# Kernel tuning notes

Hardware: AMD Instinct MI355X
Metric: run time of the kernel (lower is better)

Reference implementation:

```python
import jax, jax.numpy as jnp
import numpy as np

N, NS, C, S = 262144, 8, 32, 8  # points, nsample, out_channels, share_channels
EPS = 1e-5

def _bn(x, g, b, axes):
    m = jnp.mean(x, axis=axes, keepdims=True)
    v = jnp.mean((x - m) ** 2, axis=axes, keepdims=True)
    return g * (x - m) * jax.lax.rsqrt(v + EPS) + b

def setup_inputs() -> dict:
    key = jax.random.key(0)
    ks = jax.random.split(key, 16)
    lin = lambda k, i, o: (jax.random.normal(k, (o, i), jnp.float32) / np.sqrt(i)).astype(jnp.float32)
    return {
        'p': jax.random.normal(ks[0], (N, 3), jnp.float32) * 10.0,
        'x': jax.random.normal(ks[1], (N, C), jnp.float32),
        'idx': jax.random.randint(ks[2], (N, NS), 0, N, jnp.int32),
        'Wq': lin(ks[3], C, C), 'bq': jnp.zeros((C,), jnp.float32),
        'Wk': lin(ks[4], C, C), 'bk': jnp.zeros((C,), jnp.float32),
        'Wv': lin(ks[5], C, C), 'bv': jnp.zeros((C,), jnp.float32),
        'Wp1': lin(ks[6], 3, 3), 'bp1': jnp.zeros((3,), jnp.float32),
        'gp': jnp.ones((3,), jnp.float32), 'bp': jnp.zeros((3,), jnp.float32),
        'Wp2': lin(ks[7], 3, C), 'bp2': jnp.zeros((C,), jnp.float32),
        'gw1': jnp.ones((C,), jnp.float32), 'bw1': jnp.zeros((C,), jnp.float32),
        'Ww1': lin(ks[8], C, C // S), 'bww1': jnp.zeros((C // S,), jnp.float32),
        'gw2': jnp.ones((C // S,), jnp.float32), 'bw2': jnp.zeros((C // S,), jnp.float32),
        'Ww2': lin(ks[9], C // S, C // S), 'bww2': jnp.zeros((C // S,), jnp.float32),
    }

def reference(p, x, idx, Wq, bq, Wk, bk, Wv, bv, Wp1, bp1, gp, bp, Wp2, bp2,
              gw1, bw1, Ww1, bww1, gw2, bw2, Ww2, bww2):
    n = x.shape[0]
    q = x @ Wq.T + bq                      # (n, C)
    k = x @ Wk.T + bk
    v = x @ Wv.T + bv
    # queryandgroup: gather neighbors, relative xyz (use_xyz=True for key path)
    p_r = p[idx] - p[:, None, :]           # (n, ns, 3)
    kg = k[idx]                            # (n, ns, C)
    vg = v[idx]                            # (n, ns, C)
    # linear_p: Linear(3,3) -> BN(3) (over n, ns) -> ReLU -> Linear(3, C)
    p_r = p_r @ Wp1.T + bp1
    p_r = jax.nn.relu(_bn(p_r, gp, bp, (0, 1)))
    p_r = p_r @ Wp2.T + bp2                # (n, ns, C)
    # out_channels // mid_channels == 1, so the .view(...).sum(2) is identity
    w = kg - q[:, None, :] + p_r           # (n, ns, C)
    # linear_w: BN(C) -> ReLU -> Linear(C, C//S) -> BN(C//S) -> ReLU -> Linear
    w = jax.nn.relu(_bn(w, gw1, bw1, (0, 1)))
    w = w @ Ww1.T + bww1                   # (n, ns, C//S)
    w = jax.nn.relu(_bn(w, gw2, bw2, (0, 1)))
    w = w @ Ww2.T + bww2
    w = jax.nn.softmax(w, axis=1)          # softmax over nsample
    # grouped weighted sum: (n, ns, S, C//S) * (n, ns, 1, C//S)
    out = ((vg + p_r).reshape(n, NS, S, C // S) * w[:, :, None, :]).sum(1)
    return out.reshape(n, C)
```

## Files before the change

### kernel.cpp

```cpp
#include <hip/hip_runtime.h>
#include <hip/hip_bf16.h>

#define NPTS   262144
#define NSAMP  8
#define NPAIR  (NPTS * NSAMP)
#define EPSV   1e-5f
#define INVCNT (1.0f / (float)NPAIR)
#define GSTAT  1024

typedef __hip_bfloat16 bf16;

template <typename T> __device__ __forceinline__ float cvt(T v);
template <> __device__ __forceinline__ float cvt<float>(float v) { return v; }
template <> __device__ __forceinline__ float cvt<bf16>(bf16 v) { return __bfloat162float(v); }

template <typename T> __device__ __forceinline__ T f2t(float v);
template <> __device__ __forceinline__ float f2t<float>(float v) { return v; }
template <> __device__ __forceinline__ bf16  f2t<bf16>(float v)  { return __float2bfloat16(v); }

__global__ void k_detect(const unsigned int* __restrict__ xw, int* __restrict__ flag)
{
    if (threadIdx.x == 0 && blockIdx.x == 0) {
        int cnt = 0;
        for (int i = 0; i < 256; ++i) {
            const unsigned int w = xw[i];
            const unsigned int e = (w >> 7) & 0xFF;
            if (e >= 110 && e <= 132) ++cnt;
        }
        flag[0] = (cnt >= 128) ? 0 : 1;
    }
}

template <typename T>
__global__ __launch_bounds__(256) void k_qkv(
    const T* __restrict__ x,
    const T* __restrict__ Wq, const T* __restrict__ bq,
    const T* __restrict__ Wk, const T* __restrict__ bk,
    const T* __restrict__ Wv, const T* __restrict__ bv,
    float* __restrict__ q, float* __restrict__ k, float* __restrict__ v,
    const int* __restrict__ flag, const int want)
{
    if (flag[0] != want) return;
    __shared__ float Wt[3][32][32];
    __shared__ float xs[8][32];
    const int t = threadIdx.x;
    for (int e = t; e < 1024; e += 256) {
        const int c = e >> 5, j = e & 31;
        Wt[0][j][c] = cvt<T>(Wq[e]);
        Wt[1][j][c] = cvt<T>(Wk[e]);
        Wt[2][j][c] = cvt<T>(Wv[e]);
    }
    __syncthreads();
    const int c = t & 31, pi = t >> 5;
    const float bqv = cvt<T>(bq[c]), bkv = cvt<T>(bk[c]), bvv = cvt<T>(bv[c]);
    const int base0 = blockIdx.x * 256;
    for (int it = 0; it < 32; ++it) {
        const int base = base0 + it * 8;
        __syncthreads();
        xs[t >> 5][t & 31] = cvt<T>(x[base * 32 + t]);
        __syncthreads();
        float aq = bqv, ak = bkv, av = bvv;
#pragma unroll
        for (int j = 0; j < 32; ++j) {
            const float xv = xs[pi][j];
            aq += Wt[0][j][c] * xv;
            ak += Wt[1][j][c] * xv;
            av += Wt[2][j][c] * xv;
        }
        const int o = (base + pi) * 32 + c;
        q[o] = aq; k[o] = ak; v[o] = av;
    }
}

template <typename T>
__global__ __launch_bounds__(256) void k_pr1(
    const T* __restrict__ p, const int* __restrict__ idx,
    const T* __restrict__ Wp1, const T* __restrict__ bp1,
    float* __restrict__ pr1, float* __restrict__ P1,
    const int* __restrict__ flag, const int want)
{
    if (flag[0] != want) return;
    float W[3][3], B[3];
#pragma unroll
    for (int a = 0; a < 3; ++a) {
        B[a] = cvt<T>(bp1[a]);
#pragma unroll
        for (int d = 0; d < 3; ++d) W[a][d] = cvt<T>(Wp1[a * 3 + d]);
    }
    const int t = threadIdx.x;
    const int base = blockIdx.x * 2048;
    float s[3] = {0.f, 0.f, 0.f}, ss[3] = {0.f, 0.f, 0.f};
    for (int it = 0; it < 2048; it += 256) {
        const int pid = base + it + t;
        const int i = pid >> 3;
        const int nj = idx[pid];
        const float d0 = cvt<T>(p[nj * 3 + 0]) - cvt<T>(p[i * 3 + 0]);
        const float d1 = cvt<T>(p[nj * 3 + 1]) - cvt<T>(p[i * 3 + 1]);
        const float d2 = cvt<T>(p[nj * 3 + 2]) - cvt<T>(p[i * 3 + 2]);
#pragma unroll
        for (int a = 0; a < 3; ++a) {
            const float r = W[a][0] * d0 + W[a][1] * d1 + W[a][2] * d2 + B[a];
            pr1[pid * 3 + a] = r;
            s[a] += r; ss[a] += r * r;
        }
    }
#pragma unroll
    for (int o = 32; o > 0; o >>= 1) {
#pragma unroll
        for (int a = 0; a < 3; ++a) { s[a] += __shfl_down(s[a], o); ss[a] += __shfl_down(ss[a], o); }
    }
    __shared__ float red[4][16];
    const int wid = t >> 6, lane = t & 63;
    if (lane == 0) {
#pragma unroll
        for (int u = 0; u < 16; ++u) red[wid][u] = 0.f;
#pragma unroll
        for (int a = 0; a < 3; ++a) { red[wid][a] = s[a]; red[wid][8 + a] = ss[a]; }
    }
    __syncthreads();
    if (t < 16) P1[blockIdx.x * 16 + t] = red[0][t] + red[1][t] + red[2][t] + red[3][t];
}

template <typename T, int NC_, int NP_>
__global__ __launch_bounds__(1024) void k_fin(
    const float* __restrict__ P, const int nblocks,
    const T* __restrict__ g, const T* __restrict__ b,
    float* __restrict__ A, float* __restrict__ Cc,
    const int* __restrict__ flag, const int want)
{
    if (flag[0] != want) return;
    constexpr int COLS = 2 * NP_;
    constexpr int GRP  = 1024 / COLS;
    const int t = threadIdx.x;
    const int c = t % COLS;
    const int gi = t / COLS;
    float acc = 0.f;
    for (int r = gi; r < nblocks; r += GRP) acc += P[r * COLS + c];
    __shared__ float red[1024];
    red[t] = acc;
    __syncthreads();
#pragma unroll
    for (int s = GRP >> 1; s > 0; s >>= 1) {
        if (gi < s) red[t] += red[t + s * COLS];
        __syncthreads();
    }
    if (t < NC_) {
        const float m = red[t] * INVCNT;
        const float var = red[NP_ + t] * INVCNT - m * m;
        const float a = cvt<T>(g[t]) * rsqrtf(var + EPSV);
        A[t] = a;
        Cc[t] = cvt<T>(b[t]) - a * m;
    }
}

template <typename T>
__global__ __launch_bounds__(256) void k_bn2stat(
    const int* __restrict__ idx, const float* __restrict__ pr1,
    const float* __restrict__ q, const float* __restrict__ k,
    const T* __restrict__ Wp2, const T* __restrict__ bp2,
    const float* __restrict__ coef, float* __restrict__ P2,
    const int* __restrict__ flag, const int want)
{
    if (flag[0] != want) return;
    const int t = threadIdx.x;
    const int c = t & 31;
    const float a10 = coef[0], a11 = coef[1], a12 = coef[2];
    const float c10 = coef[8], c11 = coef[9], c12 = coef[10];
    const float w0 = cvt<T>(Wp2[c * 3 + 0]), w1 = cvt<T>(Wp2[c * 3 + 1]), w2 = cvt<T>(Wp2[c * 3 + 2]);
    const float bb = cvt<T>(bp2[c]);
    float s = 0.f, ss = 0.f;
    const int base = blockIdx.x * 2048;
    for (int it = 0; it < 2048; it += 8) {
        const int pid = base + it + (t >> 5);
        const int i = pid >> 3;
        const int nj = idx[pid];
        const float h0 = fmaxf(a10 * pr1[pid * 3 + 0] + c10, 0.f);
        const float h1 = fmaxf(a11 * pr1[pid * 3 + 1] + c11, 0.f);
        const float h2 = fmaxf(a12 * pr1[pid * 3 + 2] + c12, 0.f);
        const float pr2 = w0 * h0 + w1 * h1 + w2 * h2 + bb;
        const float wp = k[nj * 32 + c] - q[i * 32 + c] + pr2;
        s += wp; ss += wp * wp;
    }
    s += __shfl_down(s, 32); ss += __shfl_down(ss, 32);
    __shared__ float red[4][64];
    const int wid = t >> 6, lane = t & 63;
    if (lane < 32) { red[wid][lane] = s; red[wid][32 + lane] = ss; }
    __syncthreads();
    if (t < 64) P2[blockIdx.x * 64 + t] = red[0][t] + red[1][t] + red[2][t] + red[3][t];
}

template <typename T>
__global__ __launch_bounds__(256) void k_w1(
    const int* __restrict__ idx, const float* __restrict__ pr1,
    const float* __restrict__ q, const float* __restrict__ k,
    const T* __restrict__ Wp2, const T* __restrict__ bp2,
    const T* __restrict__ Ww1, const T* __restrict__ bww1,
    const float* __restrict__ coef, float* __restrict__ w1out, float* __restrict__ P3,
    const int* __restrict__ flag, const int want)
{
    if (flag[0] != want) return;
    __shared__ float sWp2[32][3], sbp2[32], sW1[4][32], sb1[4], sa2[32], sc2[32];
    const int t = threadIdx.x;
    if (t < 32) {
        sWp2[t][0] = cvt<T>(Wp2[t * 3 + 0]);
        sWp2[t][1] = cvt<T>(Wp2[t * 3 + 1]);
        sWp2[t][2] = cvt<T>(Wp2[t * 3 + 2]);
        sbp2[t] = cvt<T>(bp2[t]);
        sa2[t] = coef[16 + t];
        sc2[t] = coef[48 + t];
    }
    if (t < 4) sb1[t] = cvt<T>(bww1[t]);
    if (t < 128) sW1[t >> 5][t & 31] = cvt<T>(Ww1[t]);
    __syncthreads();
    const float a10 = coef[0], a11 = coef[1], a12 = coef[2];
    const float c10 = coef[8], c11 = coef[9], c12 = coef[10];
    float s[4] = {0.f, 0.f, 0.f, 0.f}, ss[4] = {0.f, 0.f, 0.f, 0.f};
    const int base = blockIdx.x * 2048;
    for (int it = 0; it < 2048; it += 256) {
        const int pid = base + it + t;
        const int i = pid >> 3;
        const int nj = idx[pid];
        const float h0 = fmaxf(a10 * pr1[pid * 3 + 0] + c10, 0.f);
        const float h1 = fmaxf(a11 * pr1[pid * 3 + 1] + c11, 0.f);
        const float h2 = fmaxf(a12 * pr1[pid * 3 + 2] + c12, 0.f);
        float acc[4] = {sb1[0], sb1[1], sb1[2], sb1[3]};
        const float* krow = k + nj * 32;
        const float* qrow = q + i * 32;
#pragma unroll
        for (int cc = 0; cc < 32; ++cc) {
            const float pr2 = sWp2[cc][0] * h0 + sWp2[cc][1] * h1 + sWp2[cc][2] * h2 + sbp2[cc];
            const float wp = krow[cc] - qrow[cc] + pr2;
            const float hh = fmaxf(sa2[cc] * wp + sc2[cc], 0.f);
            acc[0] += sW1[0][cc] * hh;
            acc[1] += sW1[1][cc] * hh;
            acc[2] += sW1[2][cc] * hh;
            acc[3] += sW1[3][cc] * hh;
        }
#pragma unroll
        for (int u = 0; u < 4; ++u) {
            w1out[pid * 4 + u] = acc[u];
            s[u] += acc[u]; ss[u] += acc[u] * acc[u];
        }
    }
#pragma unroll
    for (int o = 32; o > 0; o >>= 1) {
#pragma unroll
        for (int u = 0; u < 4; ++u) { s[u] += __shfl_down(s[u], o); ss[u] += __shfl_down(ss[u], o); }
    }
    __shared__ float red[4][8];
    const int wid = t >> 6, lane = t & 63;
    if (lane == 0) {
#pragma unroll
        for (int u = 0; u < 4; ++u) { red[wid][u] = s[u]; red[wid][4 + u] = ss[u]; }
    }
    __syncthreads();
    if (t < 8) P3[blockIdx.x * 8 + t] = red[0][t] + red[1][t] + red[2][t] + red[3][t];
}

template <typename T>
__global__ __launch_bounds__(256) void k_out(
    const int* __restrict__ idx, const float* __restrict__ pr1,
    const float* __restrict__ v, const float* __restrict__ w1in,
    const T* __restrict__ Wp2, const T* __restrict__ bp2,
    const T* __restrict__ Ww2, const T* __restrict__ bww2,
    const float* __restrict__ coef, T* __restrict__ out,
    const int* __restrict__ flag, const int want)
{
    if (flag[0] != want) return;
    const int t = threadIdx.x;
    const int c = t & 31, pi = t >> 5;
    const float a10 = coef[0], a11 = coef[1], a12 = coef[2];
    const float c10 = coef[8], c11 = coef[9], c12 = coef[10];
    const float wA = cvt<T>(Wp2[c * 3 + 0]), wB = cvt<T>(Wp2[c * 3 + 1]), wC = cvt<T>(Wp2[c * 3 + 2]);
    const float bb = cvt<T>(bp2[c]);
    const int tq = c & 3;
    float a3[4], c3[4], W2r[4];
#pragma unroll
    for (int u = 0; u < 4; ++u) {
        a3[u] = coef[80 + u]; c3[u] = coef[88 + u];
        W2r[u] = cvt<T>(Ww2[tq * 4 + u]);
    }
    const float b2r = cvt<T>(bww2[tq]);
    const int base0 = blockIdx.x * 256;
    for (int it = 0; it < 32; ++it) {
        const int i = base0 + it * 8 + pi;
        float lg[8];
#pragma unroll
        for (int j = 0; j < 8; ++j) {
            const float* wr = w1in + (i * 8 + j) * 4;
            float l = b2r;
#pragma unroll
            for (int u = 0; u < 4; ++u) l += W2r[u] * fmaxf(a3[u] * wr[u] + c3[u], 0.f);
            lg[j] = l;
        }
        float m = lg[0];
#pragma unroll
        for (int j = 1; j < 8; ++j) m = fmaxf(m, lg[j]);
        float sum = 0.f;
#pragma unroll
        for (int j = 0; j < 8; ++j) { lg[j] = __expf(lg[j] - m); sum += lg[j]; }
        const float inv = 1.f / sum;
        float acc = 0.f;
#pragma unroll
        for (int j = 0; j < 8; ++j) {
            const int pid = i * 8 + j;
            const int nj = idx[pid];
            const float h0 = fmaxf(a10 * pr1[pid * 3 + 0] + c10, 0.f);
            const float h1 = fmaxf(a11 * pr1[pid * 3 + 1] + c11, 0.f);
            const float h2 = fmaxf(a12 * pr1[pid * 3 + 2] + c12, 0.f);
            const float pr2 = wA * h0 + wB * h1 + wC * h2 + bb;
            acc += (v[nj * 32 + c] + pr2) * (lg[j] * inv);
        }
        out[i * 32 + c] = f2t<T>(acc);
    }
}

template <typename T>
static void launch_pipeline(void* const* d_in, void* d_out, float* ws,
                            int* flag, const int want, hipStream_t stream)
{
    const T*   p    = (const T*)d_in[0];
    const T*   x    = (const T*)d_in[1];
    const int* idx  = (const int*)d_in[2];
    const T*   Wq   = (const T*)d_in[3];
    const T*   bq   = (const T*)d_in[4];
    const T*   Wk   = (const T*)d_in[5];
    const T*   bk   = (const T*)d_in[6];
    const T*   Wv   = (const T*)d_in[7];
    const T*   bv   = (const T*)d_in[8];
    const T*   Wp1  = (const T*)d_in[9];
    const T*   bp1  = (const T*)d_in[10];
    const T*   gp   = (const T*)d_in[11];
    const T*   bp   = (const T*)d_in[12];
    const T*   Wp2  = (const T*)d_in[13];
    const T*   bp2  = (const T*)d_in[14];
    const T*   gw1  = (const T*)d_in[15];
    const T*   bw1  = (const T*)d_in[16];
    const T*   Ww1  = (const T*)d_in[17];
    const T*   bww1 = (const T*)d_in[18];
    const T*   gw2  = (const T*)d_in[19];
    const T*   bw2  = (const T*)d_in[20];
    const T*   Ww2  = (const T*)d_in[21];
    const T*   bww2 = (const T*)d_in[22];
    T* out = (T*)d_out;

    float* coef = ws + 16;
    float* P1   = ws + 128;
    float* P2   = P1 + GSTAT * 16;
    float* P3   = P2 + GSTAT * 64;
    float* q    = ws + 131072;
    float* k    = q  + (size_t)NPTS * 32;
    float* v    = k  + (size_t)NPTS * 32;
    float* pr1  = v  + (size_t)NPTS * 32;
    float* w1   = pr1 + (size_t)NPAIR * 3;

    k_qkv<T><<<1024, 256, 0, stream>>>(x, Wq, bq, Wk, bk, Wv, bv, q, k, v, flag, want);
    k_pr1<T><<<GSTAT, 256, 0, stream>>>(p, idx, Wp1, bp1, pr1, P1, flag, want);
    k_fin<T, 3, 8><<<1, 1024, 0, stream>>>(P1, GSTAT, gp, bp, coef + 0, coef + 8, flag, want);
    k_bn2stat<T><<<GSTAT, 256, 0, stream>>>(idx, pr1, q, k, Wp2, bp2, coef, P2, flag, want);
    k_fin<T, 32, 32><<<1, 1024, 0, stream>>>(P2, GSTAT, gw1, bw1, coef + 16, coef + 48, flag, want);
    k_w1<T><<<GSTAT, 256, 0, stream>>>(idx, pr1, q, k, Wp2, bp2, Ww1, bww1, coef, w1, P3, flag, want);
    k_fin<T, 4, 4><<<1, 1024, 0, stream>>>(P3, GSTAT, gw2, bw2, coef + 80, coef + 88, flag, want);
    k_out<T><<<1024, 256, 0, stream>>>(idx, pr1, v, w1, Wp2, bp2, Ww2, bww2, coef, out, flag, want);
}

extern "C" void kernel_launch(void* const* d_in, const int* in_sizes, int n_in,
                              void* d_out, int out_size, void* d_ws, size_t ws_size,
                              hipStream_t stream)
{
    float* ws = (float*)d_ws;
    int* flag = (int*)ws;

    k_detect<<<1, 64, 0, stream>>>((const unsigned int*)d_in[1], flag);
    launch_pipeline<bf16>(d_in, d_out, ws, flag, 0, stream);
    launch_pipeline<float>(d_in, d_out, ws, flag, 1, stream);
}
```

Measured before the change: 519.0 us.

## Double grid sizes to 2048 blocks and unroll bn2stat gathers by four

Doubles the block count for every per-point kernel, halving the work per block, and moves the workspace offset for q so the larger partial-stat buffers fit. k_bn2stat now issues four independent idx/pr1/k/q loads per iteration before using them, to expose more memory-level parallelism on the random gathers. Several index computations are widened to size_t. The risk is more partial sums for the single-block finalize kernels to reduce.

```diff
diff --git a/kernel.cpp b/kernel.cpp
--- a/kernel.cpp
+++ b/kernel.cpp
@@ -6,7 +6,8 @@
 #define NPAIR  (NPTS * NSAMP)
 #define EPSV   1e-5f
 #define INVCNT (1.0f / (float)NPAIR)
-#define GSTAT  1024
+#define GSTAT  2048
+#define PPB    (NPAIR / GSTAT)
 
 typedef __hip_bfloat16 bf16;
 
@@ -53,8 +54,8 @@
     __syncthreads();
     const int c = t & 31, pi = t >> 5;
     const float bqv = cvt<T>(bq[c]), bkv = cvt<T>(bk[c]), bvv = cvt<T>(bv[c]);
-    const int base0 = blockIdx.x * 256;
-    for (int it = 0; it < 32; ++it) {
+    const int base0 = blockIdx.x * 128;
+    for (int it = 0; it < 16; ++it) {
         const int base = base0 + it * 8;
         __syncthreads();
         xs[t >> 5][t & 31] = cvt<T>(x[base * 32 + t]);
@@ -88,9 +89,9 @@
         for (int d = 0; d < 3; ++d) W[a][d] = cvt<T>(Wp1[a * 3 + d]);
     }
     const int t = threadIdx.x;
-    const int base = blockIdx.x * 2048;
+    const int base = blockIdx.x * PPB;
     float s[3] = {0.f, 0.f, 0.f}, ss[3] = {0.f, 0.f, 0.f};
-    for (int it = 0; it < 2048; it += 256) {
+    for (int it = 0; it < PPB; it += 256) {
         const int pid = base + it + t;
         const int i = pid >> 3;
         const int nj = idx[pid];
@@ -164,22 +165,38 @@
     if (flag[0] != want) return;
     const int t = threadIdx.x;
     const int c = t & 31;
+    const int sub = t >> 5;
     const float a10 = coef[0], a11 = coef[1], a12 = coef[2];
     const float c10 = coef[8], c11 = coef[9], c12 = coef[10];
     const float w0 = cvt<T>(Wp2[c * 3 + 0]), w1 = cvt<T>(Wp2[c * 3 + 1]), w2 = cvt<T>(Wp2[c * 3 + 2]);
     const float bb = cvt<T>(bp2[c]);
     float s = 0.f, ss = 0.f;
-    const int base = blockIdx.x * 2048;
-    for (int it = 0; it < 2048; it += 8) {
-        const int pid = base + it + (t >> 5);
-        const int i = pid >> 3;
-        const int nj = idx[pid];
-        const float h0 = fmaxf(a10 * pr1[pid * 3 + 0] + c10, 0.f);
-        const float h1 = fmaxf(a11 * pr1[pid * 3 + 1] + c11, 0.f);
-        const float h2 = fmaxf(a12 * pr1[pid * 3 + 2] + c12, 0.f);
-        const float pr2 = w0 * h0 + w1 * h1 + w2 * h2 + bb;
-        const float wp = k[nj * 32 + c] - q[i * 32 + c] + pr2;
-        s += wp; ss += wp * wp;
+    const int base = blockIdx.x * PPB;
+    for (int it = 0; it < PPB; it += 32) {
+        int pids[4], njs[4];
+#pragma unroll
+        for (int u = 0; u < 4; ++u) pids[u] = base + it + u * 8 + sub;
+#pragma unroll
+        for (int u = 0; u < 4; ++u) njs[u] = idx[pids[u]];
+        float h[4][3];
+#pragma unroll
+        for (int u = 0; u < 4; ++u) {
+            h[u][0] = fmaxf(a10 * pr1[pids[u] * 3 + 0] + c10, 0.f);
+            h[u][1] = fmaxf(a11 * pr1[pids[u] * 3 + 1] + c11, 0.f);
+            h[u][2] = fmaxf(a12 * pr1[pids[u] * 3 + 2] + c12, 0.f);
+        }
+        float kv[4], qv[4];
+#pragma unroll
+        for (int u = 0; u < 4; ++u) {
+            kv[u] = k[(size_t)njs[u] * 32 + c];
+            qv[u] = q[(size_t)(pids[u] >> 3) * 32 + c];
+        }
+#pragma unroll
+        for (int u = 0; u < 4; ++u) {
+            const float pr2 = w0 * h[u][0] + w1 * h[u][1] + w2 * h[u][2] + bb;
+            const float wp = kv[u] - qv[u] + pr2;
+            s += wp; ss += wp * wp;
+        }
     }
     s += __shfl_down(s, 32); ss += __shfl_down(ss, 32);
     __shared__ float red[4][64];
@@ -215,8 +232,8 @@
     const float a10 = coef[0], a11 = coef[1], a12 = coef[2];
     const float c10 = coef[8], c11 = coef[9], c12 = coef[10];
     float s[4] = {0.f, 0.f, 0.f, 0.f}, ss[4] = {0.f, 0.f, 0.f, 0.f};
-    const int base = blockIdx.x * 2048;
-    for (int it = 0; it < 2048; it += 256) {
+    const int base = blockIdx.x * PPB;
+    for (int it = 0; it < PPB; it += 256) {
         const int pid = base + it + t;
         const int i = pid >> 3;
         const int nj = idx[pid];
@@ -224,8 +241,8 @@
         const float h1 = fmaxf(a11 * pr1[pid * 3 + 1] + c11, 0.f);
         const float h2 = fmaxf(a12 * pr1[pid * 3 + 2] + c12, 0.f);
         float acc[4] = {sb1[0], sb1[1], sb1[2], sb1[3]};
-        const float* krow = k + nj * 32;
-        const float* qrow = q + i * 32;
+        const float* krow = k + (size_t)nj * 32;
+        const float* qrow = q + (size_t)i * 32;
 #pragma unroll
         for (int cc = 0; cc < 32; ++cc) {
             const float pr2 = sWp2[cc][0] * h0 + sWp2[cc][1] * h1 + sWp2[cc][2] * h2 + sbp2[cc];
@@ -281,13 +298,13 @@
         W2r[u] = cvt<T>(Ww2[tq * 4 + u]);
     }
     const float b2r = cvt<T>(bww2[tq]);
-    const int base0 = blockIdx.x * 256;
-    for (int it = 0; it < 32; ++it) {
+    const int base0 = blockIdx.x * 128;
+    for (int it = 0; it < 16; ++it) {
         const int i = base0 + it * 8 + pi;
         float lg[8];
 #pragma unroll
         for (int j = 0; j < 8; ++j) {
-            const float* wr = w1in + (i * 8 + j) * 4;
+            const float* wr = w1in + ((size_t)i * 8 + j) * 4;
             float l = b2r;
 #pragma unroll
             for (int u = 0; u < 4; ++u) l += W2r[u] * fmaxf(a3[u] * wr[u] + c3[u], 0.f);
@@ -309,9 +326,9 @@
             const float h1 = fmaxf(a11 * pr1[pid * 3 + 1] + c11, 0.f);
             const float h2 = fmaxf(a12 * pr1[pid * 3 + 2] + c12, 0.f);
             const float pr2 = wA * h0 + wB * h1 + wC * h2 + bb;
-            acc += (v[nj * 32 + c] + pr2) * (lg[j] * inv);
-        }
-        out[i * 32 + c] = f2t<T>(acc);
+            acc += (v[(size_t)nj * 32 + c] + pr2) * (lg[j] * inv);
+        }
+        out[(size_t)i * 32 + c] = f2t<T>(acc);
     }
 }
 
@@ -348,20 +365,20 @@
     float* P1   = ws + 128;
     float* P2   = P1 + GSTAT * 16;
     float* P3   = P2 + GSTAT * 64;
-    float* q    = ws + 131072;
+    float* q    = ws + 262144;
     float* k    = q  + (size_t)NPTS * 32;
     float* v    = k  + (size_t)NPTS * 32;
     float* pr1  = v  + (size_t)NPTS * 32;
     float* w1   = pr1 + (size_t)NPAIR * 3;
 
-    k_qkv<T><<<1024, 256, 0, stream>>>(x, Wq, bq, Wk, bk, Wv, bv, q, k, v, flag, want);
+    k_qkv<T><<<2048, 256, 0, stream>>>(x, Wq, bq, Wk, bk, Wv, bv, q, k, v, flag, want);
     k_pr1<T><<<GSTAT, 256, 0, stream>>>(p, idx, Wp1, bp1, pr1, P1, flag, want);
     k_fin<T, 3, 8><<<1, 1024, 0, stream>>>(P1, GSTAT, gp, bp, coef + 0, coef + 8, flag, want);
     k_bn2stat<T><<<GSTAT, 256, 0, stream>>>(idx, pr1, q, k, Wp2, bp2, coef, P2, flag, want);
     k_fin<T, 32, 32><<<1, 1024, 0, stream>>>(P2, GSTAT, gw1, bw1, coef + 16, coef + 48, flag, want);
     k_w1<T><<<GSTAT, 256, 0, stream>>>(idx, pr1, q, k, Wp2, bp2, Ww1, bww1, coef, w1, P3, flag, want);
     k_fin<T, 4, 4><<<1, 1024, 0, stream>>>(P3, GSTAT, gw2, bw2, coef + 80, coef + 88, flag, want);
-    k_out<T><<<1024, 256, 0, stream>>>(idx, pr1, v, w1, Wp2, bp2, Ww2, bww2, coef, out, flag, want);
+    k_out<T><<<2048, 256, 0, stream>>>(idx, pr1, v, w1, Wp2, bp2, Ww2, bww2, coef, out, flag, want);
 }
 
 extern "C" void kernel_launch(void* const* d_in, const int* in_sizes, int n_in,
```

Result: no change. 525.1 us (+1.2%).
